# Optimization experiments

Measured on AMD Instinct MI355X. Metric: run time of the kernel, lower is better.

The kernel has to match this reference:

```python
import jax, jax.numpy as jnp
import numpy as np

N, E, P = 50000, 800000, 100000
IN, HID, H, L = 128, 128, 8, 3
D = HID // H


def setup_inputs() -> dict:
    key = jax.random.key(0)
    ks = jax.random.split(key, 24)
    rn = lambda k, shape, s: (jax.random.normal(k, shape, jnp.float32) * s)
    inp = {
        'x': jax.random.normal(ks[0], (N, IN), jnp.float32),
        'edge_src': jax.random.randint(ks[1], (E,), 0, N, jnp.int32),
        'edge_dst': jax.random.randint(ks[2], (E,), 0, N, jnp.int32),
        'edge_w': jax.random.uniform(ks[3], (E,), jnp.float32),
        'pos_src': jax.random.randint(ks[4], (P,), 0, N, jnp.int32),
        'pos_dst': jax.random.randint(ks[5], (P,), 0, N, jnp.int32),
        'neg_src': jax.random.randint(ks[6], (P,), 0, N, jnp.int32),
        'neg_dst': jax.random.randint(ks[7], (P,), 0, N, jnp.int32),
        # input projection
        'W_in': rn(ks[8], (IN, HID), IN ** -0.5),
        'b_in': jnp.zeros((HID,), jnp.float32),
        # per-layer HGT params (single ntype/etype -> plain matrices)
        'Wk': rn(ks[9], (L, HID, HID), HID ** -0.5),
        'Wq': rn(ks[10], (L, HID, HID), HID ** -0.5),
        'Wv': rn(ks[11], (L, HID, HID), HID ** -0.5),
        'att_w': rn(ks[12], (L, H, D, D), D ** -0.5),
        'msg_w': rn(ks[13], (L, H, D, D), D ** -0.5),
        'pri': jnp.ones((L, H), jnp.float32),
        'Wa': rn(ks[14], (L, HID, HID), HID ** -0.5),
        'skip': jnp.ones((L,), jnp.float32),
        # predictor MLP
        'W1': rn(ks[15], (HID, HID // 2), HID ** -0.5),
        'b1': jnp.zeros((HID // 2,), jnp.float32),
        'W2': rn(ks[16], (HID // 2, HID // 4), (HID // 2) ** -0.5),
        'b2': jnp.zeros((HID // 4,), jnp.float32),
        'W3': rn(ks[17], (HID // 4, 1), (HID // 4) ** -0.5),
        'b3': jnp.zeros((1,), jnp.float32),
    }
    return inp


def _hgt_forward(x, edge_src, edge_dst, edge_w, pos_src, pos_dst, neg_src, neg_dst,
                 W_in, b_in, Wk, Wq, Wv, att_w, msg_w, pri, Wa, skip,
                 W1, b1, W2, b2, W3, b3):
    n = x.shape[0]
    nheads = att_w.shape[1]
    d = att_w.shape[2]
    sqrt_d = jnp.asarray(d ** 0.5, x.dtype)
    h = jax.nn.relu(x @ W_in + b_in)
    nlayers = Wk.shape[0]
    for l in range(nlayers):
        k = (h @ Wk[l]).reshape(n, nheads, d)
        q = (h @ Wq[l]).reshape(n, nheads, d)
        v = (h @ Wv[l]).reshape(n, nheads, d)
        # relation-specific per-head transforms (etype constant -> node-level)
        kw = jnp.einsum('nhd,hde->nhe', k, att_w[l])
        mv = jnp.einsum('nhd,hde->nhe', v, msg_w[l])
        # per-edge attention logits [E, H]
        a = (kw[edge_src] * q[edge_dst]).sum(-1) * pri[l] / sqrt_d
        # edge softmax grouped by destination node
        amax = jax.ops.segment_max(a, edge_dst, num_segments=n)[edge_dst]
        ex = jnp.exp(a - amax)
        denom = jax.ops.segment_sum(ex, edge_dst, num_segments=n)[edge_dst]
        attn = ex / denom
        # weighted messages + scatter-sum  [E,H,D] -> [N,H,D]
        m = mv[edge_src] * edge_w[:, None, None] * attn[:, :, None]
        agg = jax.ops.segment_sum(m, edge_dst, num_segments=n).reshape(n, nheads * d)
        hn = agg @ Wa[l]  # linear_a (dropout is identity in eval)
        alpha = jax.nn.sigmoid(skip[l])
        h = hn * alpha + h * (1.0 - alpha)
        if l != nlayers - 1:
            h = jax.nn.relu(h)  # inter-layer relu (dropout identity)
    def predictor(z):
        z = jax.nn.leaky_relu(z @ W1 + b1, 0.2)
        z = jax.nn.leaky_relu(z @ W2 + b2, 0.2)
        return z @ W3 + b3
    h_pos = predictor(h[pos_src] * h[pos_dst])
    h_neg = predictor(h[neg_src] * h[neg_dst])
    return h_pos, h_neg, h


def reference(x, edge_src, edge_dst, edge_w, pos_src, pos_dst, neg_src, neg_dst,
              W_in, b_in, Wk, Wq, Wv, att_w, msg_w, pri, Wa, skip,
              W1, b1, W2, b2, W3, b3):
    return _hgt_forward(x, edge_src, edge_dst, edge_w, pos_src, pos_dst,
                        neg_src, neg_dst, W_in, b_in, Wk, Wq, Wv, att_w,
                        msg_w, pri, Wa, skip, W1, b1, W2, b2, W3, b3)
```

## Files before the change

### kernel.cpp

```cpp
#include <hip/hip_runtime.h>
#include <cstddef>

#define N_NODES 50000
#define N_EDGES 800000
#define N_PAIRS 100000

typedef float floatx4 __attribute__((ext_vector_type(4)));
typedef _Float16 half2v __attribute__((ext_vector_type(2)));
typedef _Float16 half4v __attribute__((ext_vector_type(4)));
typedef _Float16 half8v __attribute__((ext_vector_type(8)));

__device__ inline size_t packA(int m, int k, int K) {
  return ((size_t)((m >> 4) * (K >> 5) + (k >> 5)) << 9) +
         ((((unsigned)k >> 3) & 3) << 7) + ((m & 15) << 3) + (k & 7);
}
__device__ inline void store_h8(_Float16* __restrict__ dst, size_t base, const float* vals) {
  half8v hv;
#pragma unroll
  for (int i = 0; i < 8; i++) hv[i] = (_Float16)vals[i];
  *(half8v*)(dst + base) = hv;
}

__device__ inline float fold_val(int l, int r, int j, const float* Wk, const float* Wq,
                                 const float* Wv, const float* att, const float* msg,
                                 const float* pri) {
  if (j >= 128 && j < 256) return Wq[(l * 128 + r) * 128 + (j - 128)];
  int jj = j & 127, hh = jj >> 4, e = jj & 15;
  const float* W = (j < 128) ? Wk : Wv;
  const float* T = (j < 128) ? att : msg;
  float s = 0.f;
#pragma unroll
  for (int d = 0; d < 16; d++)
    s += W[(l * 128 + r) * 128 + hh * 16 + d] * T[((l * 8 + hh) * 16 + d) * 16 + e];
  if (j < 128) s *= pri[l * 8 + hh] * 0.25f;
  return s;
}

__global__ void wprep_kernel(const float* __restrict__ W_in, const float* __restrict__ Wk,
                             const float* __restrict__ Wq, const float* __restrict__ Wv,
                             const float* __restrict__ att, const float* __restrict__ msg,
                             const float* __restrict__ pri, const float* __restrict__ Wa,
                             const float* __restrict__ W1, const float* __restrict__ W2,
                             _Float16* Wint, _Float16* Wcat, _Float16* Waf,
                             _Float16* W1f, _Float16* W2f) {
  int gid = blockIdx.x * 256 + threadIdx.x;
  float v;
  _Float16* dt;
  size_t o;
  if (gid < 16384) {
    int n = gid >> 7, k = gid & 127;
    v = W_in[k * 128 + n];
    dt = Wint; o = packA(n, k, 128);
  } else if (gid < 163840) {
    int t = gid - 16384;
    int l = t / 49152, u = t - l * 49152;
    int n = u >> 7, k = u & 127;
    v = fold_val(l, k, n, Wk, Wq, Wv, att, msg, pri);
    dt = Wcat + (size_t)l * 49152;
    o = packA(n, k, 128);
  } else if (gid < 212992) {
    int t = gid - 163840;
    int l = t / 16384, u = t & 16383;
    int n = u >> 7, k = u & 127;
    v = Wa[(size_t)l * 16384 + k * 128 + n];
    dt = Waf + (size_t)l * 16384;
    o = packA(n, k, 128);
  } else if (gid < 221184) {
    int u = gid - 212992;
    int n = u >> 7, k = u & 127;
    v = W1[k * 64 + n];
    dt = W1f; o = packA(n, k, 128);
  } else if (gid < 225280) {
    int u = gid - 221184;
    int n = u >> 6, k = u & 63;
    v = (n < 32) ? W2[k * 32 + n] : 0.f;
    dt = W2f; o = packA(n, k, 64);
  } else {
    return;
  }
  dt[o] = (_Float16)v;
}

__global__ void hist_kernel(const int* __restrict__ dst, int* __restrict__ deg, int E) {
  int g = blockIdx.x * blockDim.x + threadIdx.x;
  if (g < E) atomicAdd(&deg[dst[g]], 1);
}

__global__ void scanA_kernel(const int* __restrict__ deg, int* __restrict__ offs,
                             int* __restrict__ bsum, int n) {
  __shared__ int sm[256];
  int t = threadIdx.x;
  int i = blockIdx.x * 256 + t;
  int v = (i < n) ? ((deg[i] + 15) & ~15) : 0;
  sm[t] = v;
  __syncthreads();
  for (int off = 1; off < 256; off <<= 1) {
    int u = (t >= off) ? sm[t - off] : 0;
    __syncthreads();
    sm[t] += u;
    __syncthreads();
  }
  if (i < n) offs[i] = sm[t] - v;
  if (t == 255) bsum[blockIdx.x] = sm[255];
}

__global__ void scanB_kernel(const int* __restrict__ bsum, int* __restrict__ boff,
                             int* __restrict__ offs, int nb, int n) {
  __shared__ int sm[256];
  int t = threadIdx.x;
  int v = (t < nb) ? bsum[t] : 0;
  sm[t] = v;
  __syncthreads();
  for (int off = 1; off < 256; off <<= 1) {
    int u = (t >= off) ? sm[t - off] : 0;
    __syncthreads();
    sm[t] += u;
    __syncthreads();
  }
  boff[t] = sm[t] - v;
  if (t == nb - 1) offs[n] = sm[t];
}

__global__ void scanC_kernel(int* __restrict__ offs, const int* __restrict__ boff,
                             int* __restrict__ cursor, int n) {
  int i = blockIdx.x * 256 + threadIdx.x;
  if (i < n) {
    int o = offs[i] + boff[blockIdx.x];
    offs[i] = o;
    cursor[i] = o;
  }
}

__global__ void scatter_kernel(const int* __restrict__ src, const int* __restrict__ dst,
                               const float* __restrict__ w, int* __restrict__ cursor,
                               int2* __restrict__ eld, int E) {
  int g = blockIdx.x * blockDim.x + threadIdx.x;
  if (g < E) {
    int d = dst[g];
    int p = atomicAdd(&cursor[d], 1);
    eld[p] = make_int2(src[g], __float_as_int(w[g]));
  }
}

__global__ void bhist_kernel(const int* __restrict__ deg, int* __restrict__ bh, int n) {
  __shared__ int lh[256];
  int t = threadIdx.x;
  lh[t] = 0;
  __syncthreads();
  int i = blockIdx.x * 256 + t;
  if (i < n) atomicAdd(&lh[min(deg[i], 255)], 1);
  __syncthreads();
  if (lh[t]) atomicAdd(&bh[t], lh[t]);
}
__global__ void bscan_kernel(const int* __restrict__ bh, int* __restrict__ bcur) {
  __shared__ int sm[256];
  int t = threadIdx.x;
  int v = bh[255 - t];
  sm[t] = v;
  __syncthreads();
  for (int off = 1; off < 256; off <<= 1) {
    int u = (t >= off) ? sm[t - off] : 0;
    __syncthreads();
    sm[t] += u;
    __syncthreads();
  }
  bcur[255 - t] = sm[t] - v;
}
__global__ void bscatter_kernel(const int* __restrict__ deg, int* __restrict__ bcur,
                                int* __restrict__ perm, int n) {
  __shared__ int lh[256], lbase[256];
  int t = threadIdx.x;
  lh[t] = 0;
  __syncthreads();
  int i = blockIdx.x * 256 + t;
  int b = 0, local = 0;
  if (i < n) {
    b = min(deg[i], 255);
    local = atomicAdd(&lh[b], 1);
  }
  __syncthreads();
  int cnt = lh[t];
  lbase[t] = cnt ? atomicAdd(&bcur[t], cnt) : 0;
  __syncthreads();
  if (i < n) perm[lbase[b] + local] = i;
}

template <int AMODE, int CFG>
__global__ __launch_bounds__(256) void gemm_mfma(
    const _Float16* __restrict__ Ah, const float* __restrict__ Af,
    const float* __restrict__ hsrc,
    const int* __restrict__ psrc, const int* __restrict__ pdst,
    const int* __restrict__ nsrc, const int* __restrict__ ndst,
    const _Float16* __restrict__ Bt,
    int M, int N, int K, int epi,
    const float* __restrict__ bias, const _Float16* __restrict__ hold,
    const float* __restrict__ skipv, int relu,
    float* __restrict__ Cf, _Float16* __restrict__ Ch, int Kout,
    const float* __restrict__ W3, const float* __restrict__ b3,
    float* __restrict__ outd, _Float16* __restrict__ kwmv, _Float16* __restrict__ qbuf) {
  constexpr int NCHUNK = (CFG == 2) ? 3 : 1;
  int tid = threadIdx.x;
  int wave = tid >> 6, lane = tid & 63;
  int l16 = lane & 15, q = lane >> 4;
  int m_base = (CFG == 1) ? (blockIdx.x * 256 + wave * 64)
                          : (blockIdx.x * 128 + (wave >> 1) * 64);
  int nw = (CFG == 1) ? 0 : (wave & 1) * 64;
  int kc_count = K >> 5;

  bool tv[4];
  int pa[4], pb[4], rowA[4];
  size_t a_base[4];
#pragma unroll
  for (int mt = 0; mt < 4; mt++) {
    int tile = (m_base >> 4) + mt;
    tv[mt] = (tile * 16) < M;
    if (AMODE == 0) {
      a_base[mt] = (size_t)(tv[mt] ? tile : 0) * ((size_t)kc_count << 9) + lane * 8;
    } else if (AMODE == 1) {
      rowA[mt] = min(m_base + mt * 16 + l16, M - 1);
    } else {
      int gr = min(m_base + mt * 16 + l16, M - 1);
      bool pos = gr < N_PAIRS;
      int idx = pos ? gr : gr - N_PAIRS;
      pa[mt] = pos ? psrc[idx] : nsrc[idx];
      pb[mt] = pos ? pdst[idx] : ndst[idx];
    }
  }

  half8v a[4][4];
#pragma unroll
  for (int kc = 0; kc < 4; kc++) {
    if (kc >= kc_count) break;
    int kbase = kc * 32 + q * 8;
#pragma unroll
    for (int mt = 0; mt < 4; mt++) {
      if (AMODE == 0) {
        if (tv[mt]) {
          a[mt][kc] = *(const half8v*)(Ah + a_base[mt] + (kc << 9));
        } else {
          a[mt][kc] = (half8v)(_Float16)0.f;
        }
      } else if (AMODE == 1) {
        const float* p = Af + (size_t)rowA[mt] * K + kbase;
        float4 u0 = *(const float4*)p, u1 = *(const float4*)(p + 4);
        float f[8] = {u0.x, u0.y, u0.z, u0.w, u1.x, u1.y, u1.z, u1.w};
        half8v hv;
#pragma unroll
        for (int i = 0; i < 8; i++) hv[i] = (_Float16)f[i];
        a[mt][kc] = hv;
      } else {
        const float* ra = hsrc + (size_t)pa[mt] * K + kbase;
        const float* rb = hsrc + (size_t)pb[mt] * K + kbase;
        float4 a0 = *(const float4*)ra, a1 = *(const float4*)(ra + 4);
        float4 c0 = *(const float4*)rb, c1 = *(const float4*)(rb + 4);
        float f[8] = {a0.x * c0.x, a0.y * c0.y, a0.z * c0.z, a0.w * c0.w,
                      a1.x * c1.x, a1.y * c1.y, a1.z * c1.z, a1.w * c1.w};
        half8v hv;
#pragma unroll
        for (int i = 0; i < 8; i++) hv[i] = (_Float16)f[i];
        a[mt][kc] = hv;
      }
    }
  }

  __shared__ float ldsT[4][16 * 68];
  float* myT = &ldsT[wave][0];
  float alpha = 1.f, beta = 0.f;
  if (epi == 2) {
    float sv = *skipv;
    alpha = 1.f / (1.f + __expf(-sv));
    beta = 1.f - alpha;
  }
  float b3v = (epi == 4) ? b3[0] : 0.f;
  int g = lane >> 4, mloc = lane & 15;

#pragma unroll
  for (int c = 0; c < NCHUNK; c++) {
    int nb_w = nw + c * 128;
    floatx4 acc[4][4];
#pragma unroll
    for (int i = 0; i < 4; i++)
#pragma unroll
      for (int j = 0; j < 4; j++) acc[i][j] = (floatx4){0.f, 0.f, 0.f, 0.f};
    size_t bb[4];
#pragma unroll
    for (int nt = 0; nt < 4; nt++)
      bb[nt] = (size_t)((nb_w >> 4) + nt) * ((size_t)kc_count << 9) + lane * 8;
#pragma unroll
    for (int kc = 0; kc < 4; kc++) {
      if (kc >= kc_count) break;
      half8v b[4];
#pragma unroll
      for (int nt = 0; nt < 4; nt++) b[nt] = *(const half8v*)(Bt + bb[nt] + (kc << 9));
#pragma unroll
      for (int mt = 0; mt < 4; mt++)
#pragma unroll
        for (int nt = 0; nt < 4; nt++)
          acc[mt][nt] = __builtin_amdgcn_mfma_f32_16x16x32_f16(a[mt][kc], b[nt],
                                                               acc[mt][nt], 0, 0, 0);
    }

#pragma unroll
    for (int mt = 0; mt < 4; mt++) {
      int row0 = m_base + mt * 16;
#pragma unroll
      for (int nt = 0; nt < 4; nt++)
#pragma unroll
        for (int r = 0; r < 4; r++)
          myT[(q * 4 + r) * 68 + nt * 16 + l16] = acc[mt][nt][r];
      __syncthreads();
      if (tv[mt]) {
        int row = row0 + mloc;
        float outacc = 0.f;
#pragma unroll
        for (int kc2 = 0; kc2 < 2; kc2++) {
          const float* rp = myT + mloc * 68 + kc2 * 32 + g * 8;
          floatx4 v0 = *(const floatx4*)rp;
          floatx4 v1 = *(const floatx4*)(rp + 4);
          float vals[8] = {v0[0], v0[1], v0[2], v0[3], v1[0], v1[1], v1[2], v1[3]};
          int col0 = nb_w + kc2 * 32 + g * 8;
          size_t pbase = ((size_t)((row0 >> 4) * (Kout >> 5) + (col0 >> 5)) << 9) +
                         (size_t)lane * 8;
          if (epi == 0) {
            float4 bb0 = *(const float4*)&bias[col0];
            float4 bb1 = *(const float4*)&bias[col0 + 4];
            float bbv[8] = {bb0.x, bb0.y, bb0.z, bb0.w, bb1.x, bb1.y, bb1.z, bb1.w};
#pragma unroll
            for (int j = 0; j < 8; j++) vals[j] = fmaxf(vals[j] + bbv[j], 0.f);
            store_h8(Ch, pbase, vals);
          } else if (epi == 1) {
            int region = col0 >> 7;
            if (region == 1) {
              half8v hv;
#pragma unroll
              for (int j = 0; j < 8; j++) hv[j] = (_Float16)vals[j];
              *(half8v*)&qbuf[(size_t)row * 128 + (col0 - 128)] = hv;
            } else {
              int cc = col0 & 127;
              size_t base = (size_t)row * 256 + (size_t)(cc >> 2) * 8 +
                            (region == 2 ? 4 : 0);
              half4v h0, h1;
#pragma unroll
              for (int j = 0; j < 4; j++) {
                h0[j] = (_Float16)vals[j];
                h1[j] = (_Float16)vals[j + 4];
              }
              *(half4v*)&kwmv[base] = h0;
              *(half4v*)&kwmv[base + 8] = h1;
            }
          } else if (epi == 2) {
            half8v hv = *(const half8v*)(hold + pbase);
#pragma unroll
            for (int j = 0; j < 8; j++) {
              vals[j] = alpha * vals[j] + beta * (float)hv[j];
              if (relu) vals[j] = fmaxf(vals[j], 0.f);
            }
            if (Cf) {
              *(float4*)&Cf[(size_t)row * N + col0] =
                  make_float4(vals[0], vals[1], vals[2], vals[3]);
              *(float4*)&Cf[(size_t)row * N + col0 + 4] =
                  make_float4(vals[4], vals[5], vals[6], vals[7]);
            }
            if (Ch) store_h8(Ch, pbase, vals);
          } else if (epi == 3) {
            float4 bb0 = *(const float4*)&bias[col0];
            float4 bb1 = *(const float4*)&bias[col0 + 4];
            float bbv[8] = {bb0.x, bb0.y, bb0.z, bb0.w, bb1.x, bb1.y, bb1.z, bb1.w};
#pragma unroll
            for (int j = 0; j < 8; j++) {
              float v = vals[j] + bbv[j];
              vals[j] = v > 0.f ? v : 0.2f * v;
            }
            store_h8(Ch, pbase, vals);
          } else {
            bool inb = col0 < N;
            float4 bb0 = inb ? *(const float4*)&bias[col0] : make_float4(0, 0, 0, 0);
            float4 bb1 = inb ? *(const float4*)&bias[col0 + 4] : make_float4(0, 0, 0, 0);
            float4 w0 = inb ? *(const float4*)&W3[col0] : make_float4(0, 0, 0, 0);
            float4 w1 = inb ? *(const float4*)&W3[col0 + 4] : make_float4(0, 0, 0, 0);
            float bbv[8] = {bb0.x, bb0.y, bb0.z, bb0.w, bb1.x, bb1.y, bb1.z, bb1.w};
            float ww[8] = {w0.x, w0.y, w0.z, w0.w, w1.x, w1.y, w1.z, w1.w};
#pragma unroll
            for (int j = 0; j < 8; j++) {
              float v = vals[j] + bbv[j];
              v = v > 0.f ? v : 0.2f * v;
              outacc += v * ww[j];
            }
          }
        }
        if (epi == 4) {
          outacc += __shfl_xor(outacc, 16);
          outacc += __shfl_xor(outacc, 32);
          if (lane < 16) outd[row0 + lane] = outacc + b3v;
        }
      }
      __syncthreads();
    }
  }
}

__global__ __launch_bounds__(256) void edge_agg_kernel(
    const _Float16* __restrict__ kwmv, const _Float16* __restrict__ qbuf,
    const int* __restrict__ poffs, const int2* __restrict__ eld,
    const int* __restrict__ perm,
    _Float16* __restrict__ agg, int n) {
  int wslot = blockIdx.x * 4 + (threadIdx.x >> 6);
  int lane = threadIdx.x & 63;
  int hh = lane >> 5;
  int c4 = lane & 31;
  int ch = c4 << 2;
  for (int gw = wslot; gw < n; gw += 8192) {
    int node = perm[gw];
    half4v qv = *(const half4v*)&qbuf[(size_t)node * 128 + ch];
    half2v q01 = {qv[0], qv[1]}, q23 = {qv[2], qv[3]};
    float m = -1e30f, s = 0.f;
    float a0 = 0.f, a1 = 0.f, a2 = 0.f, a3 = 0.f;
    int beg = poffs[node], end = poffs[node + 1];
    for (int j = beg; j < end; j += 16) {
      int2 e[8];
      half8v kvmv[8];
#pragma unroll
      for (int i = 0; i < 8; i++) {
        e[i] = eld[j + 2 * i + hh];
        kvmv[i] = *(const half8v*)&kwmv[(size_t)max(e[i].x, 0) * 256 + (size_t)c4 * 8];
      }
      float p[8];
#pragma unroll
      for (int i = 0; i < 8; i++) {
        half2v k01 = {kvmv[i][0], kvmv[i][1]}, k23 = {kvmv[i][2], kvmv[i][3]};
        float d = __builtin_amdgcn_fdot2(
            k01, q01, __builtin_amdgcn_fdot2(k23, q23, 0.f, false), false);
        d += __shfl_xor(d, 1);
        d += __shfl_xor(d, 2);
        p[i] = (e[i].x >= 0) ? d : -1e30f;
      }
      float nm = m;
#pragma unroll
      for (int i = 0; i < 8; i++) nm = fmaxf(nm, p[i]);
      float sc = __expf(m - nm);
      float t[8];
      float ssum = 0.f;
#pragma unroll
      for (int i = 0; i < 8; i++) {
        t[i] = __expf(p[i] - nm);
        ssum += t[i];
      }
      s = s * sc + ssum;
      a0 *= sc; a1 *= sc; a2 *= sc; a3 *= sc;
#pragma unroll
      for (int i = 0; i < 8; i++) {
        float w = (e[i].x >= 0) ? __int_as_float(e[i].y) : 0.f;
        float f = t[i] * w;
        a0 += f * (float)kvmv[i][4];
        a1 += f * (float)kvmv[i][5];
        a2 += f * (float)kvmv[i][6];
        a3 += f * (float)kvmv[i][7];
      }
      m = nm;
    }
    float mo = __shfl_xor(m, 32);
    float so = __shfl_xor(s, 32);
    float c0 = __shfl_xor(a0, 32), c1 = __shfl_xor(a1, 32);
    float c2 = __shfl_xor(a2, 32), c3 = __shfl_xor(a3, 32);
    float M = fmaxf(m, mo);
    float e1 = __expf(m - M), e2 = __expf(mo - M);
    float st = s * e1 + so * e2;
    float v0 = a0 * e1 + c0 * e2, v1 = a1 * e1 + c1 * e2;
    float v2 = a2 * e1 + c2 * e2, v3 = a3 * e1 + c3 * e2;
    float inv = (st > 0.f) ? 1.f / st : 0.f;
    if (hh == 0) {
      half4v out4;
      out4[0] = (_Float16)(v0 * inv);
      out4[1] = (_Float16)(v1 * inv);
      out4[2] = (_Float16)(v2 * inv);
      out4[3] = (_Float16)(v3 * inv);
      *(half4v*)&agg[packA(node, ch, 128)] = out4;
    }
  }
}

extern "C" void kernel_launch(void* const* d_in, const int* in_sizes, int n_in,
                              void* d_out, int out_size, void* d_ws, size_t ws_size,
                              hipStream_t stream) {
  const float* x        = (const float*)d_in[0];
  const int*   edge_src = (const int*)d_in[1];
  const int*   edge_dst = (const int*)d_in[2];
  const float* edge_w   = (const float*)d_in[3];
  const int*   pos_src  = (const int*)d_in[4];
  const int*   pos_dst  = (const int*)d_in[5];
  const int*   neg_src  = (const int*)d_in[6];
  const int*   neg_dst  = (const int*)d_in[7];
  const float* W_in     = (const float*)d_in[8];
  const float* b_in     = (const float*)d_in[9];
  const float* Wk       = (const float*)d_in[10];
  const float* Wq       = (const float*)d_in[11];
  const float* Wv       = (const float*)d_in[12];
  const float* att_w    = (const float*)d_in[13];
  const float* msg_w    = (const float*)d_in[14];
  const float* pri      = (const float*)d_in[15];
  const float* Wa       = (const float*)d_in[16];
  const float* skip     = (const float*)d_in[17];
  const float* W1       = (const float*)d_in[18];
  const float* b1       = (const float*)d_in[19];
  const float* W2       = (const float*)d_in[20];
  const float* b2       = (const float*)d_in[21];
  const float* W3       = (const float*)d_in[22];
  const float* b3       = (const float*)d_in[23];
  float* out = (float*)d_out;

  char* W = (char*)d_ws;
  _Float16*  qbuf   = (_Float16*)(W + 0);
  _Float16*  kwmv   = (_Float16*)(W + 12800000);
  _Float16*  hbuf   = (_Float16*)(W + 38400000);
  _Float16*  agg    = (_Float16*)(W + 51200000);
  _Float16*  Wint   = (_Float16*)(W + 64000000);
  _Float16*  Wcat   = (_Float16*)(W + 64032768);
  _Float16*  Waf    = (_Float16*)(W + 64327680);
  _Float16*  W1f    = (_Float16*)(W + 64425984);
  _Float16*  W2f    = (_Float16*)(W + 64442368);
  int2*      eld    = (int2*)(W + 64450560);
  int*       deg    = (int*)(W + 77250560);
  int*       poffs  = (int*)(W + 77450560);
  int*       cursor = (int*)(W + 77650576);
  int*       perm   = (int*)(W + 77850576);
  int*       bsum   = (int*)(W + 78050576);
  int*       boff   = (int*)(W + 78051600);
  int*       bh     = (int*)(W + 78052624);
  int*       bcur   = (int*)(W + 78053648);
  _Float16* T1 = (_Float16*)(W + 0);
  float* hfinal = out + 2 * N_PAIRS;

  hipMemsetAsync(deg, 0, N_NODES * sizeof(int), stream);
  hipMemsetAsync(bh, 0, 1024, stream);
  hipMemsetAsync(eld, 0xFF, 12800000, stream);

  wprep_kernel<<<880, 256, 0, stream>>>(W_in, Wk, Wq, Wv, att_w, msg_w, pri, Wa, W1, W2,
                                        Wint, Wcat, Waf, W1f, W2f);
  hist_kernel<<<(N_EDGES + 255) / 256, 256, 0, stream>>>(edge_dst, deg, N_EDGES);
  scanA_kernel<<<196, 256, 0, stream>>>(deg, poffs, bsum, N_NODES);
  scanB_kernel<<<1, 256, 0, stream>>>(bsum, boff, poffs, 196, N_NODES);
  scanC_kernel<<<196, 256, 0, stream>>>(poffs, boff, cursor, N_NODES);
  scatter_kernel<<<(N_EDGES + 255) / 256, 256, 0, stream>>>(
      edge_src, edge_dst, edge_w, cursor, eld, N_EDGES);
  bhist_kernel<<<196, 256, 0, stream>>>(deg, bh, N_NODES);
  bscan_kernel<<<1, 256, 0, stream>>>(bh, bcur);
  bscatter_kernel<<<196, 256, 0, stream>>>(deg, bcur, perm, N_NODES);

  gemm_mfma<1, 0><<<dim3(391, 1), 256, 0, stream>>>(
      nullptr, x, nullptr, nullptr, nullptr, nullptr, nullptr,
      Wint, N_NODES, 128, 128, 0, b_in, nullptr, nullptr, 0,
      nullptr, hbuf, 128, nullptr, nullptr, nullptr, nullptr, nullptr);

  for (int l = 0; l < 3; l++) {
    gemm_mfma<0, 2><<<dim3(391, 1), 256, 0, stream>>>(
        hbuf, nullptr, nullptr, nullptr, nullptr, nullptr, nullptr,
        Wcat + l * 49152, N_NODES, 384, 128, 1, nullptr, nullptr, nullptr, 0,
        nullptr, nullptr, 128, nullptr, nullptr, nullptr, kwmv, qbuf);
    edge_agg_kernel<<<2048, 256, 0, stream>>>(
        kwmv, qbuf, poffs, eld, perm, agg, N_NODES);
    int last = (l == 2);
    gemm_mfma<0, 0><<<dim3(391, 1), 256, 0, stream>>>(
        agg, nullptr, nullptr, nullptr, nullptr, nullptr, nullptr,
        Waf + l * 16384, N_NODES, 128, 128, 2, nullptr, hbuf, skip + l,
        last ? 0 : 1, last ? hfinal : nullptr, last ? nullptr : hbuf, 128,
        nullptr, nullptr, nullptr, nullptr, nullptr);
  }

  gemm_mfma<2, 1><<<dim3(782, 1), 256, 0, stream>>>(
      nullptr, nullptr, hfinal, pos_src, pos_dst, neg_src, neg_dst,
      W1f, 2 * N_PAIRS, 64, 128, 3, b1, nullptr, nullptr, 0,
      nullptr, T1, 64, nullptr, nullptr, nullptr, nullptr, nullptr);
  gemm_mfma<0, 1><<<dim3(782, 1), 256, 0, stream>>>(
      T1, nullptr, nullptr, nullptr, nullptr, nullptr, nullptr,
      W2f, 2 * N_PAIRS, 32, 64, 4, b2, nullptr, nullptr, 0,
      nullptr, nullptr, 64, W3, b3, out, nullptr, nullptr);
}
```

Baseline: 622.2 us.

## Retile MFMA GEMM to 128x64 blocks over a 2D grid, fp16 pair gather

The GEMM kernel drops its per-config templates. It now uses one 128-row by 64-column tile per block on a 2D grid, with each wave owning 32 rows and 64 columns. This gives many more blocks and lower register pressure, aimed at better occupancy and load balance across the CUs. The last layer also writes a row-major fp16 copy of h, which the predictor gathers instead of the fp32 output, halving gather bytes at some precision cost. The final predictor layer does its W3 dot product with in-register shuffles instead of an LDS transpose. A side effect is that A tiles are reloaded once for each column block.

```diff
diff --git a/kernel.cpp b/kernel.cpp
--- a/kernel.cpp
+++ b/kernel.cpp
@@ -185,10 +185,10 @@
   if (i < n) perm[lbase[b] + local] = i;
 }
 
-template <int AMODE, int CFG>
+template <int AMODE>
 __global__ __launch_bounds__(256) void gemm_mfma(
     const _Float16* __restrict__ Ah, const float* __restrict__ Af,
-    const float* __restrict__ hsrc,
+    const _Float16* __restrict__ hrow_src,
     const int* __restrict__ psrc, const int* __restrict__ pdst,
     const int* __restrict__ nsrc, const int* __restrict__ ndst,
     const _Float16* __restrict__ Bt,
@@ -197,21 +197,20 @@
     const float* __restrict__ skipv, int relu,
     float* __restrict__ Cf, _Float16* __restrict__ Ch, int Kout,
     const float* __restrict__ W3, const float* __restrict__ b3,
-    float* __restrict__ outd, _Float16* __restrict__ kwmv, _Float16* __restrict__ qbuf) {
-  constexpr int NCHUNK = (CFG == 2) ? 3 : 1;
+    float* __restrict__ outd, _Float16* __restrict__ kwmv, _Float16* __restrict__ qbuf,
+    _Float16* __restrict__ hrow_out) {
   int tid = threadIdx.x;
   int wave = tid >> 6, lane = tid & 63;
   int l16 = lane & 15, q = lane >> 4;
-  int m_base = (CFG == 1) ? (blockIdx.x * 256 + wave * 64)
-                          : (blockIdx.x * 128 + (wave >> 1) * 64);
-  int nw = (CFG == 1) ? 0 : (wave & 1) * 64;
+  int m_base = blockIdx.x * 128 + wave * 32;
+  int n_base = blockIdx.y * 64;
   int kc_count = K >> 5;
 
-  bool tv[4];
-  int pa[4], pb[4], rowA[4];
-  size_t a_base[4];
-#pragma unroll
-  for (int mt = 0; mt < 4; mt++) {
+  bool tv[2];
+  int pa[2], pb[2], rowA[2];
+  size_t a_base[2];
+#pragma unroll
+  for (int mt = 0; mt < 2; mt++) {
     int tile = (m_base >> 4) + mt;
     tv[mt] = (tile * 16) < M;
     if (AMODE == 0) {
@@ -227,19 +226,16 @@
     }
   }
 
-  half8v a[4][4];
+  half8v a[2][4];
 #pragma unroll
   for (int kc = 0; kc < 4; kc++) {
     if (kc >= kc_count) break;
     int kbase = kc * 32 + q * 8;
 #pragma unroll
-    for (int mt = 0; mt < 4; mt++) {
+    for (int mt = 0; mt < 2; mt++) {
       if (AMODE == 0) {
-        if (tv[mt]) {
-          a[mt][kc] = *(const half8v*)(Ah + a_base[mt] + (kc << 9));
-        } else {
-          a[mt][kc] = (half8v)(_Float16)0.f;
-        }
+        a[mt][kc] = tv[mt] ? *(const half8v*)(Ah + a_base[mt] + (kc << 9))
+                           : (half8v)(_Float16)0.f;
       } else if (AMODE == 1) {
         const float* p = Af + (size_t)rowA[mt] * K + kbase;
         float4 u0 = *(const float4*)p, u1 = *(const float4*)(p + 4);
@@ -249,18 +245,67 @@
         for (int i = 0; i < 8; i++) hv[i] = (_Float16)f[i];
         a[mt][kc] = hv;
       } else {
-        const float* ra = hsrc + (size_t)pa[mt] * K + kbase;
-        const float* rb = hsrc + (size_t)pb[mt] * K + kbase;
-        float4 a0 = *(const float4*)ra, a1 = *(const float4*)(ra + 4);
-        float4 c0 = *(const float4*)rb, c1 = *(const float4*)(rb + 4);
-        float f[8] = {a0.x * c0.x, a0.y * c0.y, a0.z * c0.z, a0.w * c0.w,
-                      a1.x * c1.x, a1.y * c1.y, a1.z * c1.z, a1.w * c1.w};
-        half8v hv;
-#pragma unroll
-        for (int i = 0; i < 8; i++) hv[i] = (_Float16)f[i];
-        a[mt][kc] = hv;
-      }
-    }
+        half8v ha = *(const half8v*)(hrow_src + (size_t)pa[mt] * 128 + kbase);
+        half8v hb = *(const half8v*)(hrow_src + (size_t)pb[mt] * 128 + kbase);
+        a[mt][kc] = ha * hb;
+      }
+    }
+  }
+
+  floatx4 acc[2][4];
+#pragma unroll
+  for (int i = 0; i < 2; i++)
+#pragma unroll
+    for (int j = 0; j < 4; j++) acc[i][j] = (floatx4){0.f, 0.f, 0.f, 0.f};
+  size_t bb[4];
+#pragma unroll
+  for (int nt = 0; nt < 4; nt++)
+    bb[nt] = (size_t)((n_base >> 4) + nt) * ((size_t)kc_count << 9) + lane * 8;
+#pragma unroll
+  for (int kc = 0; kc < 4; kc++) {
+    if (kc >= kc_count) break;
+    half8v b[4];
+#pragma unroll
+    for (int nt = 0; nt < 4; nt++) b[nt] = *(const half8v*)(Bt + bb[nt] + (kc << 9));
+#pragma unroll
+    for (int mt = 0; mt < 2; mt++)
+#pragma unroll
+      for (int nt = 0; nt < 4; nt++)
+        acc[mt][nt] = __builtin_amdgcn_mfma_f32_16x16x32_f16(a[mt][kc], b[nt],
+                                                             acc[mt][nt], 0, 0, 0);
+  }
+
+  if (epi == 4) {
+    float b3v = b3[0];
+    float bw[4], wv[4];
+#pragma unroll
+    for (int nt = 0; nt < 4; nt++) {
+      int col = n_base + nt * 16 + l16;
+      bool inb = col < N;
+      bw[nt] = inb ? bias[col] : 0.f;
+      wv[nt] = inb ? W3[col] : 0.f;
+    }
+#pragma unroll
+    for (int mt = 0; mt < 2; mt++) {
+      if (!tv[mt]) continue;
+#pragma unroll
+      for (int r = 0; r < 4; r++) {
+        float partial = 0.f;
+#pragma unroll
+        for (int nt = 0; nt < 4; nt++) {
+          float v = acc[mt][nt][r] + bw[nt];
+          v = v > 0.f ? v : 0.2f * v;
+          partial += v * wv[nt];
+        }
+        partial += __shfl_xor(partial, 1);
+        partial += __shfl_xor(partial, 2);
+        partial += __shfl_xor(partial, 4);
+        partial += __shfl_xor(partial, 8);
+        int row = m_base + mt * 16 + q * 4 + r;
+        if (l16 == 0 && row < M) outd[row] = partial + b3v;
+      }
+    }
+    return;
   }
 
   __shared__ float ldsT[4][16 * 68];
@@ -271,131 +316,83 @@
     alpha = 1.f / (1.f + __expf(-sv));
     beta = 1.f - alpha;
   }
-  float b3v = (epi == 4) ? b3[0] : 0.f;
   int g = lane >> 4, mloc = lane & 15;
-
-#pragma unroll
-  for (int c = 0; c < NCHUNK; c++) {
-    int nb_w = nw + c * 128;
-    floatx4 acc[4][4];
-#pragma unroll
-    for (int i = 0; i < 4; i++)
-#pragma unroll
-      for (int j = 0; j < 4; j++) acc[i][j] = (floatx4){0.f, 0.f, 0.f, 0.f};
-    size_t bb[4];
+#pragma unroll
+  for (int mt = 0; mt < 2; mt++) {
+    int row0 = m_base + mt * 16;
 #pragma unroll
     for (int nt = 0; nt < 4; nt++)
-      bb[nt] = (size_t)((nb_w >> 4) + nt) * ((size_t)kc_count << 9) + lane * 8;
-#pragma unroll
-    for (int kc = 0; kc < 4; kc++) {
-      if (kc >= kc_count) break;
-      half8v b[4];
-#pragma unroll
-      for (int nt = 0; nt < 4; nt++) b[nt] = *(const half8v*)(Bt + bb[nt] + (kc << 9));
-#pragma unroll
-      for (int mt = 0; mt < 4; mt++)
-#pragma unroll
-        for (int nt = 0; nt < 4; nt++)
-          acc[mt][nt] = __builtin_amdgcn_mfma_f32_16x16x32_f16(a[mt][kc], b[nt],
-                                                               acc[mt][nt], 0, 0, 0);
-    }
-
-#pragma unroll
-    for (int mt = 0; mt < 4; mt++) {
-      int row0 = m_base + mt * 16;
-#pragma unroll
-      for (int nt = 0; nt < 4; nt++)
-#pragma unroll
-        for (int r = 0; r < 4; r++)
-          myT[(q * 4 + r) * 68 + nt * 16 + l16] = acc[mt][nt][r];
-      __syncthreads();
-      if (tv[mt]) {
-        int row = row0 + mloc;
-        float outacc = 0.f;
-#pragma unroll
-        for (int kc2 = 0; kc2 < 2; kc2++) {
-          const float* rp = myT + mloc * 68 + kc2 * 32 + g * 8;
-          floatx4 v0 = *(const floatx4*)rp;
-          floatx4 v1 = *(const floatx4*)(rp + 4);
-          float vals[8] = {v0[0], v0[1], v0[2], v0[3], v1[0], v1[1], v1[2], v1[3]};
-          int col0 = nb_w + kc2 * 32 + g * 8;
-          size_t pbase = ((size_t)((row0 >> 4) * (Kout >> 5) + (col0 >> 5)) << 9) +
-                         (size_t)lane * 8;
-          if (epi == 0) {
-            float4 bb0 = *(const float4*)&bias[col0];
-            float4 bb1 = *(const float4*)&bias[col0 + 4];
-            float bbv[8] = {bb0.x, bb0.y, bb0.z, bb0.w, bb1.x, bb1.y, bb1.z, bb1.w};
-#pragma unroll
-            for (int j = 0; j < 8; j++) vals[j] = fmaxf(vals[j] + bbv[j], 0.f);
-            store_h8(Ch, pbase, vals);
-          } else if (epi == 1) {
-            int region = col0 >> 7;
-            if (region == 1) {
-              half8v hv;
-#pragma unroll
-              for (int j = 0; j < 8; j++) hv[j] = (_Float16)vals[j];
-              *(half8v*)&qbuf[(size_t)row * 128 + (col0 - 128)] = hv;
-            } else {
-              int cc = col0 & 127;
-              size_t base = (size_t)row * 256 + (size_t)(cc >> 2) * 8 +
-                            (region == 2 ? 4 : 0);
-              half4v h0, h1;
-#pragma unroll
-              for (int j = 0; j < 4; j++) {
-                h0[j] = (_Float16)vals[j];
-                h1[j] = (_Float16)vals[j + 4];
-              }
-              *(half4v*)&kwmv[base] = h0;
-              *(half4v*)&kwmv[base + 8] = h1;
+#pragma unroll
+      for (int r = 0; r < 4; r++)
+        myT[(q * 4 + r) * 68 + nt * 16 + l16] = acc[mt][nt][r];
+    __syncthreads();
+    if (tv[mt]) {
+      int row = row0 + mloc;
+#pragma unroll
+      for (int kc2 = 0; kc2 < 2; kc2++) {
+        const float* rp = myT + mloc * 68 + kc2 * 32 + g * 8;
+        floatx4 v0 = *(const floatx4*)rp;
+        floatx4 v1 = *(const floatx4*)(rp + 4);
+        float vals[8] = {v0[0], v0[1], v0[2], v0[3], v1[0], v1[1], v1[2], v1[3]};
+        int col0 = n_base + kc2 * 32 + g * 8;
+        size_t pbase = ((size_t)((row0 >> 4) * (Kout >> 5) + (col0 >> 5)) << 9) +
+                       (size_t)lane * 8;
+        if (epi == 0) {
+          float4 bb0 = *(const float4*)&bias[col0];
+          float4 bb1 = *(const float4*)&bias[col0 + 4];
+          float bbv[8] = {bb0.x, bb0.y, bb0.z, bb0.w, bb1.x, bb1.y, bb1.z, bb1.w};
+#pragma unroll
+          for (int j = 0; j < 8; j++) vals[j] = fmaxf(vals[j] + bbv[j], 0.f);
+          store_h8(Ch, pbase, vals);
+        } else if (epi == 1) {
+          int region = col0 >> 7;
+          if (region == 1) {
+            half8v hv;
+#pragma unroll
+            for (int j = 0; j < 8; j++) hv[j] = (_Float16)vals[j];
+            *(half8v*)&qbuf[(size_t)row * 128 + (col0 - 128)] = hv;
+          } else {
+            int cc = col0 & 127;
+            size_t base = (size_t)row * 256 + (size_t)(cc >> 2) * 8 +
+                          (region == 2 ? 4 : 0);
+            half4v h0, h1;
+#pragma unroll
+            for (int j = 0; j < 4; j++) {
+              h0[j] = (_Float16)vals[j];
+              h1[j] = (_Float16)vals[j + 4];
             }
-          } else if (epi == 2) {
-            half8v hv = *(const half8v*)(hold + pbase);
-#pragma unroll
-            for (int j = 0; j < 8; j++) {
-              vals[j] = alpha * vals[j] + beta * (float)hv[j];
-              if (relu) vals[j] = fmaxf(vals[j], 0.f);
-            }
-            if (Cf) {
-              *(float4*)&Cf[(size_t)row * N + col0] =
-                  make_float4(vals[0], vals[1], vals[2], vals[3]);
-              *(float4*)&Cf[(size_t)row * N + col0 + 4] =
-                  make_float4(vals[4], vals[5], vals[6], vals[7]);
-            }
-            if (Ch) store_h8(Ch, pbase, vals);
-          } else if (epi == 3) {
-            float4 bb0 = *(const float4*)&bias[col0];
-            float4 bb1 = *(const float4*)&bias[col0 + 4];
-            float bbv[8] = {bb0.x, bb0.y, bb0.z, bb0.w, bb1.x, bb1.y, bb1.z, bb1.w};
-#pragma unroll
-            for (int j = 0; j < 8; j++) {
-              float v = vals[j] + bbv[j];
-              vals[j] = v > 0.f ? v : 0.2f * v;
-            }
-            store_h8(Ch, pbase, vals);
-          } else {
-            bool inb = col0 < N;
-            float4 bb0 = inb ? *(const float4*)&bias[col0] : make_float4(0, 0, 0, 0);
-            float4 bb1 = inb ? *(const float4*)&bias[col0 + 4] : make_float4(0, 0, 0, 0);
-            float4 w0 = inb ? *(const float4*)&W3[col0] : make_float4(0, 0, 0, 0);
-            float4 w1 = inb ? *(const float4*)&W3[col0 + 4] : make_float4(0, 0, 0, 0);
-            float bbv[8] = {bb0.x, bb0.y, bb0.z, bb0.w, bb1.x, bb1.y, bb1.z, bb1.w};
-            float ww[8] = {w0.x, w0.y, w0.z, w0.w, w1.x, w1.y, w1.z, w1.w};
-#pragma unroll
-            for (int j = 0; j < 8; j++) {
-              float v = vals[j] + bbv[j];
-              v = v > 0.f ? v : 0.2f * v;
-              outacc += v * ww[j];
-            }
+            *(half4v*)&kwmv[base] = h0;
+            *(half4v*)&kwmv[base + 8] = h1;
           }
+        } else if (epi == 2) {
+          half8v hv = *(const half8v*)(hold + pbase);
+#pragma unroll
+          for (int j = 0; j < 8; j++) {
+            vals[j] = alpha * vals[j] + beta * (float)hv[j];
+            if (relu) vals[j] = fmaxf(vals[j], 0.f);
+          }
+          if (Cf) {
+            *(float4*)&Cf[(size_t)row * N + col0] =
+                make_float4(vals[0], vals[1], vals[2], vals[3]);
+            *(float4*)&Cf[(size_t)row * N + col0 + 4] =
+                make_float4(vals[4], vals[5], vals[6], vals[7]);
+          }
+          if (Ch) store_h8(Ch, pbase, vals);
+          if (hrow_out) store_h8(hrow_out, (size_t)row * 128 + col0, vals);
+        } else {
+          float4 bb0 = *(const float4*)&bias[col0];
+          float4 bb1 = *(const float4*)&bias[col0 + 4];
+          float bbv[8] = {bb0.x, bb0.y, bb0.z, bb0.w, bb1.x, bb1.y, bb1.z, bb1.w};
+#pragma unroll
+          for (int j = 0; j < 8; j++) {
+            float v = vals[j] + bbv[j];
+            vals[j] = v > 0.f ? v : 0.2f * v;
+          }
+          store_h8(Ch, pbase, vals);
         }
-        if (epi == 4) {
-          outacc += __shfl_xor(outacc, 16);
-          outacc += __shfl_xor(outacc, 32);
-          if (lane < 16) outd[row0 + lane] = outacc + b3v;
-        }
-      }
-      __syncthreads();
-    }
+      }
+    }
+    __syncthreads();
   }
 }
 
@@ -527,6 +524,7 @@
   int*       boff   = (int*)(W + 78051600);
   int*       bh     = (int*)(W + 78052624);
   int*       bcur   = (int*)(W + 78053648);
+  _Float16*  hrow   = (_Float16*)(W + 78054912);
   _Float16* T1 = (_Float16*)(W + 0);
   float* hfinal = out + 2 * N_PAIRS;
 
@@ -546,32 +544,32 @@
   bscan_kernel<<<1, 256, 0, stream>>>(bh, bcur);
   bscatter_kernel<<<196, 256, 0, stream>>>(deg, bcur, perm, N_NODES);
 
-  gemm_mfma<1, 0><<<dim3(391, 1), 256, 0, stream>>>(
+  gemm_mfma<1><<<dim3(391, 2), 256, 0, stream>>>(
       nullptr, x, nullptr, nullptr, nullptr, nullptr, nullptr,
       Wint, N_NODES, 128, 128, 0, b_in, nullptr, nullptr, 0,
-      nullptr, hbuf, 128, nullptr, nullptr, nullptr, nullptr, nullptr);
+      nullptr, hbuf, 128, nullptr, nullptr, nullptr, nullptr, nullptr, nullptr);
 
   for (int l = 0; l < 3; l++) {
-    gemm_mfma<0, 2><<<dim3(391, 1), 256, 0, stream>>>(
+    gemm_mfma<0><<<dim3(391, 6), 256, 0, stream>>>(
         hbuf, nullptr, nullptr, nullptr, nullptr, nullptr, nullptr,
         Wcat + l * 49152, N_NODES, 384, 128, 1, nullptr, nullptr, nullptr, 0,
-        nullptr, nullptr, 128, nullptr, nullptr, nullptr, kwmv, qbuf);
+        nullptr, nullptr, 128, nullptr, nullptr, nullptr, kwmv, qbuf, nullptr);
     edge_agg_kernel<<<2048, 256, 0, stream>>>(
         kwmv, qbuf, poffs, eld, perm, agg, N_NODES);
     int last = (l == 2);
-    gemm_mfma<0, 0><<<dim3(391, 1), 256, 0, stream>>>(
+    gemm_mfma<0><<<dim3(391, 2), 256, 0, stream>>>(
         agg, nullptr, nullptr, nullptr, nullptr, nullptr, nullptr,
         Waf + l * 16384, N_NODES, 128, 128, 2, nullptr, hbuf, skip + l,
         last ? 0 : 1, last ? hfinal : nullptr, last ? nullptr : hbuf, 128,
-        nullptr, nullptr, nullptr, nullptr, nullptr);
-  }
-
-  gemm_mfma<2, 1><<<dim3(782, 1), 256, 0, stream>>>(
-      nullptr, nullptr, hfinal, pos_src, pos_dst, neg_src, neg_dst,
+        nullptr, nullptr, nullptr, nullptr, nullptr, last ? hrow : nullptr);
+  }
+
+  gemm_mfma<2><<<dim3(1563, 1), 256, 0, stream>>>(
+      nullptr, nullptr, hrow, pos_src, pos_dst, neg_src, neg_dst,
       W1f, 2 * N_PAIRS, 64, 128, 3, b1, nullptr, nullptr, 0,
-      nullptr, T1, 64, nullptr, nullptr, nullptr, nullptr, nullptr);
-  gemm_mfma<0, 1><<<dim3(782, 1), 256, 0, stream>>>(
+      nullptr, T1, 64, nullptr, nullptr, nullptr, nullptr, nullptr, nullptr);
+  gemm_mfma<0><<<dim3(1563, 1), 256, 0, stream>>>(
       T1, nullptr, nullptr, nullptr, nullptr, nullptr, nullptr,
       W2f, 2 * N_PAIRS, 32, 64, 4, b2, nullptr, nullptr, 0,
-      nullptr, nullptr, 64, W3, b3, out, nullptr, nullptr);
-}
+      nullptr, nullptr, 64, W3, b3, out, nullptr, nullptr, nullptr);
+}
```

After: 602.4 us. 3.2% less time.
